# Kernel tuning notes

Hardware: AMD Instinct MI355X
Metric: run time of the kernel (lower is better)

## Reference

```python
import jax, jax.numpy as jnp
import numpy as np

B, S, E, U = 4, 512, 512, 256

def setup_inputs() -> dict:
    key = jax.random.key(0)
    k1, k2, k3, k4 = jax.random.split(key, 4)
    h1 = jax.random.normal(k1, (B, S, E), dtype=jnp.float32)
    h2 = jax.random.normal(k2, (B, S, E), dtype=jnp.float32)
    # glorot-ish scaled weights
    w = jax.random.normal(k3, (2 * E, U), dtype=jnp.float32) * (2.0 / (2 * E + U)) ** 0.5
    b1 = jnp.zeros((U,), dtype=jnp.float32)
    v = jax.random.normal(k4, (U, 1), dtype=jnp.float32) * (2.0 / (U + 1)) ** 0.5
    b2 = jnp.zeros((1,), dtype=jnp.float32)
    return {"h1": h1, "h2": h2, "w": w, "b1": b1, "v": v, "b2": b2}

def reference(h1, h2, w, b1, v, b2):
    # Original: for each query step i, concat([h1, repeat(h2[:,i])]) @ w.
    # Split w so the concat-matmul becomes two separate projections:
    #   concat([h1_j, h2_i]) @ w == h1_j @ w1 + h2_i @ w2
    E_ = h1.shape[-1]
    w1, w2 = w[:E_], w[E_:]
    key_pre = jnp.einsum('bje,eu->bju', h1, w1)   # [B,Sk,U]
    qry_pre = jnp.einsum('bie,eu->biu', h2, w2)   # [B,Sq,U]
    # energy: [B,Sq,Sk,U]
    t = jnp.tanh(qry_pre[:, :, None, :] + key_pre[:, None, :, :] + b1)
    scores = jnp.einsum('biju,uo->bij', t, v) + b2[0]  # [B,Sq,Sk]
    p = jax.nn.softmax(scores, axis=-1)                # softmax over keys j
    # context per query: sum_j p[b,i,j] * h1[b,j]
    return jnp.einsum('bij,bje->bie', p, h1)           # [B,S,E]
```

## Files before the change

### kernel.cpp

```cpp
#include <hip/hip_runtime.h>
#include <hip/hip_bf16.h>

#define B_ 4
#define S_ 512
#define E_ 512
#define U_ 256

#define KC 2.885390081777927f

#if __has_builtin(__builtin_amdgcn_exp2f)
#define EXP2F(x) __builtin_amdgcn_exp2f(x)
#else
#define EXP2F(x) __exp2f(x)
#endif
#if __has_builtin(__builtin_amdgcn_rcpf)
#define RCPF(x) __builtin_amdgcn_rcpf(x)
#else
#define RCPF(x) (1.0f / (x))
#endif

typedef __attribute__((ext_vector_type(8))) short bf16x8;
typedef __attribute__((ext_vector_type(4))) float f32x4;

__device__ __forceinline__ unsigned short bf16rn(float x) {
    unsigned int u = __float_as_uint(x);
    u = (u + 0x7FFFu + ((u >> 16) & 1u)) >> 16;
    return (unsigned short)u;
}
__device__ __forceinline__ void splitT(float x, short* hi, short* lo) {
    const unsigned u = __float_as_uint(x);
    *hi = (short)(u >> 16);
    const float hf = __uint_as_float(u & 0xFFFF0000u);
    *lo = (short)(__float_as_uint(x - hf) >> 16);
}

__global__ __launch_bounds__(256) void prep_kernel(
    const float* __restrict__ w, const float* __restrict__ h1,
    bf16x8* __restrict__ whi, bf16x8* __restrict__ wlo,
    bf16x8* __restrict__ h1c)
{
    const int t = blockIdx.x * 256 + threadIdx.x;
    if (t < 32768) {
        const int lane = t & 63, kc = (t >> 6) & 15, nt = (t >> 10) & 15, z = t >> 14;
        const int quad = lane >> 4, l16 = lane & 15;
        const float* __restrict__ src =
            w + (size_t)z * E_ * U_ + (size_t)(kc * 32 + quad * 8) * U_ + nt * 16 + l16;
        bf16x8 hi, lo;
#pragma unroll
        for (int j = 0; j < 8; ++j) {
            short h, l; splitT(src[(size_t)j * U_] * KC, &h, &l);
            hi[j] = h; lo[j] = l;
        }
        whi[t] = hi; wlo[t] = lo;
    } else {
        const int s = t - 32768;
        const int lane = s & 63, kc = (s >> 6) & 15, et = (s >> 10) & 31, b = s >> 15;
        const int quad = lane >> 4, l16 = lane & 15;
        const float* __restrict__ src =
            h1 + ((size_t)b * S_ + kc * 32 + quad * 8) * E_ + et * 16 + l16;
        bf16x8 c;
#pragma unroll
        for (int j = 0; j < 8; ++j)
            c[j] = (short)bf16rn(src[(size_t)j * E_]);
        h1c[s] = c;
    }
}

__global__ __launch_bounds__(256) void gemm_pre(
    const float* __restrict__ h1, const float* __restrict__ h2,
    const bf16x8* __restrict__ whi, const bf16x8* __restrict__ wlo,
    const float* __restrict__ b1,
    float* __restrict__ keySt, float* __restrict__ qryS)
{
    const int tid = threadIdx.x;
    const int wv = tid >> 6, lane = tid & 63;
    const int quad = lane >> 4, l16 = lane & 15;
    const int wt = blockIdx.x * 4 + wv;
    const int z = wt >> 9, rem = wt & 511;
    const int m0 = (rem >> 2) << 4;
    const int ng = rem & 3;

    const float* __restrict__ Arow = (z ? h2 : h1) + (size_t)(m0 + l16) * E_;
    const bf16x8* __restrict__ Wh = whi + ((z * 16 + ng * 4) * 16) * 64 + lane;
    const bf16x8* __restrict__ Wl = wlo + ((z * 16 + ng * 4) * 16) * 64 + lane;

    f32x4 acc[4];
#pragma unroll
    for (int i = 0; i < 4; ++i) acc[i] = (f32x4){0.f, 0.f, 0.f, 0.f};

    for (int kc = 0; kc < 16; ++kc) {
        const int kb = kc * 32 + quad * 8;
        const float4 x0 = *(const float4*)&Arow[kb];
        const float4 x1 = *(const float4*)&Arow[kb + 4];
        const float xs[8] = {x0.x, x0.y, x0.z, x0.w, x1.x, x1.y, x1.z, x1.w};
        bf16x8 ah, al;
#pragma unroll
        for (int j = 0; j < 8; ++j) {
            short h, l; splitT(xs[j], &h, &l);
            ah[j] = h; al[j] = l;
        }
#pragma unroll
        for (int nt = 0; nt < 4; ++nt) {
            const bf16x8 bh = Wh[(nt * 16 + kc) * 64];
            const bf16x8 bl = Wl[(nt * 16 + kc) * 64];
            acc[nt] = __builtin_amdgcn_mfma_f32_16x16x32_bf16(ah, bh, acc[nt], 0, 0, 0);
            acc[nt] = __builtin_amdgcn_mfma_f32_16x16x32_bf16(ah, bl, acc[nt], 0, 0, 0);
            acc[nt] = __builtin_amdgcn_mfma_f32_16x16x32_bf16(al, bh, acc[nt], 0, 0, 0);
        }
    }

    if (z == 0) {
        const int b = m0 >> 9;
        const int j0 = (m0 & (S_ - 1)) + quad * 4;
#pragma unroll
        for (int nt = 0; nt < 4; ++nt) {
            const int u = (ng * 4 + nt) * 16 + l16;
            *(float4*)&keySt[((size_t)b * U_ + u) * S_ + j0] =
                make_float4(acc[nt][0], acc[nt][1], acc[nt][2], acc[nt][3]);
        }
    } else {
        const int row = m0 + quad * 4;
#pragma unroll
        for (int nt = 0; nt < 4; ++nt) {
            const int u = (ng * 4 + nt) * 16 + l16;
            const float bias = KC * b1[u];
#pragma unroll
            for (int r = 0; r < 4; ++r)
                qryS[(size_t)(row + r) * U_ + u] = acc[nt][r] + bias;
        }
    }
}

__device__ __forceinline__ float quadTerm(float a0, float a1, float a2, float a3,
                                          float4 vq, float acc) {
    const float F1 = EXP2F(a0) + 1.f;
    const float F2 = EXP2F(a1) + 1.f;
    const float F3 = EXP2F(a2) + 1.f;
    const float F4 = EXP2F(a3) + 1.f;
    const float P12 = F1 * F2, P34 = F3 * F4;
    const float n12 = fmaf(vq.y, F1, vq.x * F2);
    const float n34 = fmaf(vq.w, F3, vq.z * F4);
    const float num = fmaf(n34, P12, n12 * P34);
    return fmaf(num, RCPF(P12 * P34), acc);
}

__global__ __launch_bounds__(256) void scores_kernel(
    const float* __restrict__ keySt, const float* __restrict__ qryS,
    const float* __restrict__ v, unsigned short* __restrict__ Pp)
{
    const int i0 = blockIdx.x * 2;
    const int b = blockIdx.y;
    const int tid = threadIdx.x;
    const int wv = tid >> 6;

    __shared__ float ssm[4][2];

    const float* __restrict__ q0p = qryS + ((size_t)b * S_ + i0) * U_;
    const float4* __restrict__ q0v = (const float4*)q0p;
    const float4* __restrict__ q1v = (const float4*)(q0p + U_);
    const float4* __restrict__ vv4 = (const float4*)v;
    const float2* __restrict__ kb2 =
        (const float2*)(keySt + (size_t)b * U_ * S_) + tid;

    float a00 = 0.f, a01 = 0.f, a10 = 0.f, a11 = 0.f;
#pragma unroll 2
    for (int ub = 0; ub < U_ / 4; ++ub) {
        const float4 q0 = q0v[ub], q1 = q1v[ub], vq = vv4[ub];
        const float2 k0 = kb2[(ub * 4 + 0) * (S_ / 2)];
        const float2 k1 = kb2[(ub * 4 + 1) * (S_ / 2)];
        const float2 k2 = kb2[(ub * 4 + 2) * (S_ / 2)];
        const float2 k3 = kb2[(ub * 4 + 3) * (S_ / 2)];
        a00 = quadTerm(q0.x + k0.x, q0.y + k1.x, q0.z + k2.x, q0.w + k3.x, vq, a00);
        a01 = quadTerm(q0.x + k0.y, q0.y + k1.y, q0.z + k2.y, q0.w + k3.y, vq, a01);
        a10 = quadTerm(q1.x + k0.x, q1.y + k1.x, q1.z + k2.x, q1.w + k3.x, vq, a10);
        a11 = quadTerm(q1.x + k0.y, q1.y + k1.y, q1.z + k2.y, q1.w + k3.y, vq, a11);
    }

    const float p00 = EXP2F(-a00 * KC), p01 = EXP2F(-a01 * KC);
    const float p10 = EXP2F(-a10 * KC), p11 = EXP2F(-a11 * KC);
    float s0 = p00 + p01, s1 = p10 + p11;
#pragma unroll
    for (int off = 1; off < 64; off <<= 1) {
        s0 += __shfl_xor(s0, off, 64);
        s1 += __shfl_xor(s1, off, 64);
    }
    if ((tid & 63) == 0) { ssm[wv][0] = s0; ssm[wv][1] = s1; }
    __syncthreads();
    s0 = (ssm[0][0] + ssm[1][0]) + (ssm[2][0] + ssm[3][0]);
    s1 = (ssm[0][1] + ssm[1][1]) + (ssm[2][1] + ssm[3][1]);
    const float r0 = RCPF(s0), r1 = RCPF(s1);

    const int j2 = tid * 2;
    const int itile = i0 >> 4;
    const int base = (itile * 16 + (j2 >> 5)) * 64 + (((j2 >> 3) & 3) << 4);
    const int eo = tid & 3;
    unsigned* __restrict__ Pu = (unsigned*)(Pp + (size_t)b * S_ * S_);
    const unsigned w0 = (unsigned)bf16rn(p00 * r0) | ((unsigned)bf16rn(p01 * r0) << 16);
    const unsigned w1 = (unsigned)bf16rn(p10 * r1) | ((unsigned)bf16rn(p11 * r1) << 16);
    Pu[(base + (i0 & 15)) * 4 + eo] = w0;
    Pu[(base + ((i0 + 1) & 15)) * 4 + eo] = w1;
}

__global__ __launch_bounds__(256) void pv_gemm(
    const unsigned short* __restrict__ Pp, const bf16x8* __restrict__ h1c,
    float* __restrict__ out)
{
    const int tid = threadIdx.x;
    const int wv = tid >> 6, lane = tid & 63;
    const int quad = lane >> 4, l16 = lane & 15;
    const int wt = blockIdx.x * 4 + wv;
    const int b = wt >> 8, rem = wt & 255;
    const int it = rem >> 3, eg = rem & 7;

    const bf16x8* __restrict__ Ab =
        (const bf16x8*)(Pp + (size_t)b * S_ * S_) + (it * 16) * 64 + lane;
    const bf16x8* __restrict__ Bb =
        h1c + ((b * 32 + eg * 4) * 16) * 64 + lane;

    f32x4 acc[4];
#pragma unroll
    for (int i = 0; i < 4; ++i) acc[i] = (f32x4){0.f, 0.f, 0.f, 0.f};

    for (int kc = 0; kc < 16; ++kc) {
        const bf16x8 a8 = Ab[kc * 64];
#pragma unroll
        for (int n = 0; n < 4; ++n) {
            const bf16x8 b8 = Bb[(n * 16 + kc) * 64];
            acc[n] = __builtin_amdgcn_mfma_f32_16x16x32_bf16(a8, b8, acc[n], 0, 0, 0);
        }
    }

    const int i = it * 16 + quad * 4;
#pragma unroll
    for (int n = 0; n < 4; ++n) {
        const int e = (eg * 4 + n) * 16 + l16;
        float* __restrict__ ob = out + ((size_t)b * S_ + i) * E_ + e;
#pragma unroll
        for (int r = 0; r < 4; ++r)
            ob[(size_t)r * E_] = acc[n][r];
    }
}

extern "C" void kernel_launch(void* const* d_in, const int* in_sizes, int n_in,
                              void* d_out, int out_size, void* d_ws, size_t ws_size,
                              hipStream_t stream) {
    const float* h1 = (const float*)d_in[0];
    const float* h2 = (const float*)d_in[1];
    const float* w  = (const float*)d_in[2];
    const float* b1 = (const float*)d_in[3];
    const float* v  = (const float*)d_in[4];
    float* out = (float*)d_out;

    char* ws = (char*)d_ws;
    float* keySt = (float*)ws;                               ws += 2u << 20;
    float* qryS  = (float*)ws;                               ws += 2u << 20;
    unsigned short* Pp = (unsigned short*)ws;                ws += 2u << 20;
    bf16x8* whi = (bf16x8*)ws;                               ws += 512u << 10;
    bf16x8* wlo = (bf16x8*)ws;                               ws += 512u << 10;
    bf16x8* h1c = (bf16x8*)ws;

    prep_kernel<<<dim3(640), dim3(256), 0, stream>>>(w, h1, whi, wlo, h1c);
    gemm_pre<<<dim3(256), dim3(256), 0, stream>>>(h1, h2, whi, wlo, b1, keySt, qryS);
    scores_kernel<<<dim3(S_ / 2, B_), dim3(256), 0, stream>>>(keySt, qryS, v, Pp);
    pv_gemm<<<dim3(256), dim3(256), 0, stream>>>(Pp, h1c, out);
}
```

Measured before the change: 141.8 us.

## Fuse weight prep into projection GEMM and widen scores blocks to one key per thread

Merges the weight-split prep kernel with the projection GEMM: each block converts its slice of w into hi/lo bf16 fragments in shared memory and then runs MFMAs from LDS, dropping one launch and the global whi/wlo round trip. The h1 bf16 conversion moves to extra blocks of the same launch, and the grid is reshaped to 512 GEMM blocks with two n-tiles per wave. Separately, the scores kernel now uses 512 threads with one key per thread instead of two, which raises parallelism but writes individual shorts instead of packed words. Each GEMM block redundantly recomputes its w slice, adding conversion work.

```diff
diff --git a/kernel.cpp b/kernel.cpp
--- a/kernel.cpp
+++ b/kernel.cpp
@@ -34,26 +34,87 @@
     *lo = (short)(__float_as_uint(x - hf) >> 16);
 }
 
-__global__ __launch_bounds__(256) void prep_kernel(
-    const float* __restrict__ w, const float* __restrict__ h1,
-    bf16x8* __restrict__ whi, bf16x8* __restrict__ wlo,
+__global__ __launch_bounds__(256) void prep_gemm(
+    const float* __restrict__ h1, const float* __restrict__ h2,
+    const float* __restrict__ w, const float* __restrict__ b1,
+    float* __restrict__ keySt, float* __restrict__ qryS,
     bf16x8* __restrict__ h1c)
 {
-    const int t = blockIdx.x * 256 + threadIdx.x;
-    if (t < 32768) {
-        const int lane = t & 63, kc = (t >> 6) & 15, nt = (t >> 10) & 15, z = t >> 14;
+    __shared__ unsigned short WhiL[2][16][64][8];
+    __shared__ unsigned short WloL[2][16][64][8];
+
+    const int tid = threadIdx.x;
+    const int bid = blockIdx.x;
+
+    if (bid < 512) {
+        const int z = bid >> 8, ngg = (bid >> 5) & 7, mq = bid & 31;
+
+        const int r8 = tid >> 5, ul = tid & 31;
+        const int ntc = ul >> 4, l16c = ul & 15;
+        const float* __restrict__ Wp = w + (size_t)z * E_ * U_ + ngg * 32 + ul;
+#pragma unroll 4
+        for (int it = 0; it < 64; ++it) {
+            const int k = it * 8 + r8;
+            short h, l;
+            splitT(Wp[(size_t)k * U_] * KC, &h, &l);
+            const int kc = k >> 5, quad = (k >> 3) & 3, jj = k & 7;
+            WhiL[ntc][kc][quad * 16 + l16c][jj] = (unsigned short)h;
+            WloL[ntc][kc][quad * 16 + l16c][jj] = (unsigned short)l;
+        }
+        __syncthreads();
+
+        const int wv = tid >> 6, lane = tid & 63;
         const int quad = lane >> 4, l16 = lane & 15;
-        const float* __restrict__ src =
-            w + (size_t)z * E_ * U_ + (size_t)(kc * 32 + quad * 8) * U_ + nt * 16 + l16;
-        bf16x8 hi, lo;
-#pragma unroll
-        for (int j = 0; j < 8; ++j) {
-            short h, l; splitT(src[(size_t)j * U_] * KC, &h, &l);
-            hi[j] = h; lo[j] = l;
-        }
-        whi[t] = hi; wlo[t] = lo;
+        const int m0 = (mq * 4 + wv) * 16;
+        const float* __restrict__ Arow = (z ? h2 : h1) + (size_t)(m0 + l16) * E_;
+
+        f32x4 acc[2];
+        acc[0] = (f32x4){0.f, 0.f, 0.f, 0.f};
+        acc[1] = (f32x4){0.f, 0.f, 0.f, 0.f};
+
+        for (int kc = 0; kc < 16; ++kc) {
+            const int kb = kc * 32 + quad * 8;
+            const float4 x0 = *(const float4*)&Arow[kb];
+            const float4 x1 = *(const float4*)&Arow[kb + 4];
+            const float xs[8] = {x0.x, x0.y, x0.z, x0.w, x1.x, x1.y, x1.z, x1.w};
+            bf16x8 ah, al;
+#pragma unroll
+            for (int j = 0; j < 8; ++j) {
+                short h, l; splitT(xs[j], &h, &l);
+                ah[j] = h; al[j] = l;
+            }
+#pragma unroll
+            for (int nt = 0; nt < 2; ++nt) {
+                const bf16x8 bh = *(const bf16x8*)&WhiL[nt][kc][lane][0];
+                const bf16x8 bl = *(const bf16x8*)&WloL[nt][kc][lane][0];
+                acc[nt] = __builtin_amdgcn_mfma_f32_16x16x32_bf16(ah, bh, acc[nt], 0, 0, 0);
+                acc[nt] = __builtin_amdgcn_mfma_f32_16x16x32_bf16(ah, bl, acc[nt], 0, 0, 0);
+                acc[nt] = __builtin_amdgcn_mfma_f32_16x16x32_bf16(al, bh, acc[nt], 0, 0, 0);
+            }
+        }
+
+        if (z == 0) {
+            const int b = m0 >> 9;
+            const int j0 = (m0 & (S_ - 1)) + quad * 4;
+#pragma unroll
+            for (int nt = 0; nt < 2; ++nt) {
+                const int u = (ngg * 2 + nt) * 16 + l16;
+                *(float4*)&keySt[((size_t)b * U_ + u) * S_ + j0] =
+                    make_float4(acc[nt][0], acc[nt][1], acc[nt][2], acc[nt][3]);
+            }
+        } else {
+            const int row = m0 + quad * 4;
+#pragma unroll
+            for (int nt = 0; nt < 2; ++nt) {
+                const int u = (ngg * 2 + nt) * 16 + l16;
+                const float bias = KC * b1[u];
+#pragma unroll
+                for (int r = 0; r < 4; ++r)
+                    qryS[(size_t)(row + r) * U_ + u] = acc[nt][r] + bias;
+            }
+        }
     } else {
-        const int s = t - 32768;
+        const int s = (bid - 512) * 256 + tid;
         const int lane = s & 63, kc = (s >> 6) & 15, et = (s >> 10) & 31, b = s >> 15;
         const int quad = lane >> 4, l16 = lane & 15;
         const float* __restrict__ src =
@@ -63,71 +124,6 @@
         for (int j = 0; j < 8; ++j)
             c[j] = (short)bf16rn(src[(size_t)j * E_]);
         h1c[s] = c;
-    }
-}
-
-__global__ __launch_bounds__(256) void gemm_pre(
-    const float* __restrict__ h1, const float* __restrict__ h2,
-    const bf16x8* __restrict__ whi, const bf16x8* __restrict__ wlo,
-    const float* __restrict__ b1,
-    float* __restrict__ keySt, float* __restrict__ qryS)
-{
-    const int tid = threadIdx.x;
-    const int wv = tid >> 6, lane = tid & 63;
-    const int quad = lane >> 4, l16 = lane & 15;
-    const int wt = blockIdx.x * 4 + wv;
-    const int z = wt >> 9, rem = wt & 511;
-    const int m0 = (rem >> 2) << 4;
-    const int ng = rem & 3;
-
-    const float* __restrict__ Arow = (z ? h2 : h1) + (size_t)(m0 + l16) * E_;
-    const bf16x8* __restrict__ Wh = whi + ((z * 16 + ng * 4) * 16) * 64 + lane;
-    const bf16x8* __restrict__ Wl = wlo + ((z * 16 + ng * 4) * 16) * 64 + lane;
-
-    f32x4 acc[4];
-#pragma unroll
-    for (int i = 0; i < 4; ++i) acc[i] = (f32x4){0.f, 0.f, 0.f, 0.f};
-
-    for (int kc = 0; kc < 16; ++kc) {
-        const int kb = kc * 32 + quad * 8;
-        const float4 x0 = *(const float4*)&Arow[kb];
-        const float4 x1 = *(const float4*)&Arow[kb + 4];
-        const float xs[8] = {x0.x, x0.y, x0.z, x0.w, x1.x, x1.y, x1.z, x1.w};
-        bf16x8 ah, al;
-#pragma unroll
-        for (int j = 0; j < 8; ++j) {
-            short h, l; splitT(xs[j], &h, &l);
-            ah[j] = h; al[j] = l;
-        }
-#pragma unroll
-        for (int nt = 0; nt < 4; ++nt) {
-            const bf16x8 bh = Wh[(nt * 16 + kc) * 64];
-            const bf16x8 bl = Wl[(nt * 16 + kc) * 64];
-            acc[nt] = __builtin_amdgcn_mfma_f32_16x16x32_bf16(ah, bh, acc[nt], 0, 0, 0);
-            acc[nt] = __builtin_amdgcn_mfma_f32_16x16x32_bf16(ah, bl, acc[nt], 0, 0, 0);
-            acc[nt] = __builtin_amdgcn_mfma_f32_16x16x32_bf16(al, bh, acc[nt], 0, 0, 0);
-        }
-    }
-
-    if (z == 0) {
-        const int b = m0 >> 9;
-        const int j0 = (m0 & (S_ - 1)) + quad * 4;
-#pragma unroll
-        for (int nt = 0; nt < 4; ++nt) {
-            const int u = (ng * 4 + nt) * 16 + l16;
-            *(float4*)&keySt[((size_t)b * U_ + u) * S_ + j0] =
-                make_float4(acc[nt][0], acc[nt][1], acc[nt][2], acc[nt][3]);
-        }
-    } else {
-        const int row = m0 + quad * 4;
-#pragma unroll
-        for (int nt = 0; nt < 4; ++nt) {
-            const int u = (ng * 4 + nt) * 16 + l16;
-            const float bias = KC * b1[u];
-#pragma unroll
-            for (int r = 0; r < 4; ++r)
-                qryS[(size_t)(row + r) * U_ + u] = acc[nt][r] + bias;
-        }
     }
 }
 
@@ -144,61 +140,55 @@
     return fmaf(num, RCPF(P12 * P34), acc);
 }
 
-__global__ __launch_bounds__(256) void scores_kernel(
+__global__ __launch_bounds__(512) void scores_kernel(
     const float* __restrict__ keySt, const float* __restrict__ qryS,
     const float* __restrict__ v, unsigned short* __restrict__ Pp)
 {
     const int i0 = blockIdx.x * 2;
     const int b = blockIdx.y;
-    const int tid = threadIdx.x;
-    const int wv = tid >> 6;
-
-    __shared__ float ssm[4][2];
+    const int t = threadIdx.x;
+    const int wv = t >> 6;
+
+    __shared__ float ssm[8][2];
 
     const float* __restrict__ q0p = qryS + ((size_t)b * S_ + i0) * U_;
     const float4* __restrict__ q0v = (const float4*)q0p;
     const float4* __restrict__ q1v = (const float4*)(q0p + U_);
     const float4* __restrict__ vv4 = (const float4*)v;
-    const float2* __restrict__ kb2 =
-        (const float2*)(keySt + (size_t)b * U_ * S_) + tid;
-
-    float a00 = 0.f, a01 = 0.f, a10 = 0.f, a11 = 0.f;
-#pragma unroll 2
+    const float* __restrict__ kb = keySt + (size_t)b * U_ * S_ + t;
+
+    float a0 = 0.f, a1 = 0.f;
+#pragma unroll 4
     for (int ub = 0; ub < U_ / 4; ++ub) {
         const float4 q0 = q0v[ub], q1 = q1v[ub], vq = vv4[ub];
-        const float2 k0 = kb2[(ub * 4 + 0) * (S_ / 2)];
-        const float2 k1 = kb2[(ub * 4 + 1) * (S_ / 2)];
-        const float2 k2 = kb2[(ub * 4 + 2) * (S_ / 2)];
-        const float2 k3 = kb2[(ub * 4 + 3) * (S_ / 2)];
-        a00 = quadTerm(q0.x + k0.x, q0.y + k1.x, q0.z + k2.x, q0.w + k3.x, vq, a00);
-        a01 = quadTerm(q0.x + k0.y, q0.y + k1.y, q0.z + k2.y, q0.w + k3.y, vq, a01);
-        a10 = quadTerm(q1.x + k0.x, q1.y + k1.x, q1.z + k2.x, q1.w + k3.x, vq, a10);
-        a11 = quadTerm(q1.x + k0.y, q1.y + k1.y, q1.z + k2.y, q1.w + k3.y, vq, a11);
-    }
-
-    const float p00 = EXP2F(-a00 * KC), p01 = EXP2F(-a01 * KC);
-    const float p10 = EXP2F(-a10 * KC), p11 = EXP2F(-a11 * KC);
-    float s0 = p00 + p01, s1 = p10 + p11;
+        const float k0 = kb[(size_t)(ub * 4 + 0) * S_];
+        const float k1 = kb[(size_t)(ub * 4 + 1) * S_];
+        const float k2 = kb[(size_t)(ub * 4 + 2) * S_];
+        const float k3 = kb[(size_t)(ub * 4 + 3) * S_];
+        a0 = quadTerm(q0.x + k0, q0.y + k1, q0.z + k2, q0.w + k3, vq, a0);
+        a1 = quadTerm(q1.x + k0, q1.y + k1, q1.z + k2, q1.w + k3, vq, a1);
+    }
+
+    const float p0 = EXP2F(-a0 * KC);
+    const float p1 = EXP2F(-a1 * KC);
+    float s0 = p0, s1 = p1;
 #pragma unroll
     for (int off = 1; off < 64; off <<= 1) {
         s0 += __shfl_xor(s0, off, 64);
         s1 += __shfl_xor(s1, off, 64);
     }
-    if ((tid & 63) == 0) { ssm[wv][0] = s0; ssm[wv][1] = s1; }
+    if ((t & 63) == 0) { ssm[wv][0] = s0; ssm[wv][1] = s1; }
     __syncthreads();
-    s0 = (ssm[0][0] + ssm[1][0]) + (ssm[2][0] + ssm[3][0]);
-    s1 = (ssm[0][1] + ssm[1][1]) + (ssm[2][1] + ssm[3][1]);
+    s0 = ssm[0][0]; s1 = ssm[0][1];
+#pragma unroll
+    for (int k = 1; k < 8; ++k) { s0 += ssm[k][0]; s1 += ssm[k][1]; }
     const float r0 = RCPF(s0), r1 = RCPF(s1);
 
-    const int j2 = tid * 2;
     const int itile = i0 >> 4;
-    const int base = (itile * 16 + (j2 >> 5)) * 64 + (((j2 >> 3) & 3) << 4);
-    const int eo = tid & 3;
-    unsigned* __restrict__ Pu = (unsigned*)(Pp + (size_t)b * S_ * S_);
-    const unsigned w0 = (unsigned)bf16rn(p00 * r0) | ((unsigned)bf16rn(p01 * r0) << 16);
-    const unsigned w1 = (unsigned)bf16rn(p10 * r1) | ((unsigned)bf16rn(p11 * r1) << 16);
-    Pu[(base + (i0 & 15)) * 4 + eo] = w0;
-    Pu[(base + ((i0 + 1) & 15)) * 4 + eo] = w1;
+    const int base = (itile * 16 + (t >> 5)) * 64 + (((t >> 3) & 3) << 4);
+    unsigned short* __restrict__ pb = Pp + (size_t)b * S_ * S_;
+    pb[((base + (i0 & 15)) << 3) + (t & 7)] = bf16rn(p0 * r0);
+    pb[((base + ((i0 + 1) & 15)) << 3) + (t & 7)] = bf16rn(p1 * r1);
 }
 
 __global__ __launch_bounds__(256) void pv_gemm(
@@ -252,15 +242,12 @@
     float* out = (float*)d_out;
 
     char* ws = (char*)d_ws;
-    float* keySt = (float*)ws;                               ws += 2u << 20;
-    float* qryS  = (float*)ws;                               ws += 2u << 20;
-    unsigned short* Pp = (unsigned short*)ws;                ws += 2u << 20;
-    bf16x8* whi = (bf16x8*)ws;                               ws += 512u << 10;
-    bf16x8* wlo = (bf16x8*)ws;                               ws += 512u << 10;
+    float* keySt = (float*)ws;                 ws += 2u << 20;
+    float* qryS  = (float*)ws;                 ws += 2u << 20;
+    unsigned short* Pp = (unsigned short*)ws;  ws += 2u << 20;
     bf16x8* h1c = (bf16x8*)ws;
 
-    prep_kernel<<<dim3(640), dim3(256), 0, stream>>>(w, h1, whi, wlo, h1c);
-    gemm_pre<<<dim3(256), dim3(256), 0, stream>>>(h1, h2, whi, wlo, b1, keySt, qryS);
-    scores_kernel<<<dim3(S_ / 2, B_), dim3(256), 0, stream>>>(keySt, qryS, v, Pp);
+    prep_gemm<<<dim3(1024), dim3(256), 0, stream>>>(h1, h2, w, b1, keySt, qryS, h1c);
+    scores_kernel<<<dim3(S_ / 2, B_), dim3(512), 0, stream>>>(keySt, qryS, v, Pp);
     pv_gemm<<<dim3(256), dim3(256), 0, stream>>>(Pp, h1c, out);
 }
```

Measured after the change: 139.6 us. No clear change (-1.6%).
